# Performance work log

Hardware: AMD Instinct MI355X
Metric: run time of the kernel (lower is better)

Reference implementation:

```python
import jax, jax.numpy as jnp
import numpy as np

K = 3
STRIDE = 1
PAD = 1


def setup_inputs() -> dict:
    key = jax.random.key(0)
    k1, k2, k3 = jax.random.split(key, 3)
    N, C, H, W = 4, 256, 64, 64
    outC = 256
    x = jax.random.normal(k1, (N, C, H, W), dtype=jnp.float32)
    # offset/mask conv params (torch inits these to 0; small random makes the test nontrivial)
    conv_offset_w = jax.random.normal(k2, (3 * K * K, C, K, K), dtype=jnp.float32) * 0.01
    conv_offset_b = jnp.zeros((3 * K * K,), dtype=jnp.float32)
    # xavier-normal scale for dcn weight
    fan = C * K * K + outC * K * K
    dcn_weight = jax.random.normal(k3, (outC, C, K, K), dtype=jnp.float32) * np.float32(np.sqrt(2.0 / fan))
    return {"x": x, "conv_offset_w": conv_offset_w, "conv_offset_b": conv_offset_b, "dcn_weight": dcn_weight}


def _dcn(x, w_off, b_off, dcn_weight):
    k, s, p = K, STRIDE, PAD
    N, C, H, W = x.shape
    outC = dcn_weight.shape[0]
    KK = k * k
    # offset/mask prediction conv
    om = jax.lax.conv_general_dilated(
        x, w_off, (s, s), [(p, p), (p, p)],
        dimension_numbers=("NCHW", "OIHW", "NCHW")) + b_off[None, :, None, None]
    offset = om[:, : 2 * KK]
    mask = jax.nn.sigmoid(om[:, 2 * KK:])
    oH = (H + 2 * p - (k - 1)) // s
    oW = (W + 2 * p - (k - 1)) // s
    # pad with an extra row/col at bottom-right so floor+1 indexing is in-bounds (as in torch code)
    px = jnp.pad(x, ((0, 0), (0, 0), (p, p + 1), (p, p + 1)))
    px = jnp.transpose(px, (0, 2, 3, 1))  # (N, H+2p+1, W+2p+1, C)
    offset = jnp.transpose(offset, (0, 2, 3, 1)).reshape(N, oH, oW, KK, 2)  # (...,(y,x))
    mask = jnp.transpose(mask, (0, 2, 3, 1))  # (N, oH, oW, KK)
    base_y = jnp.arange(oH, dtype=jnp.float32) * s + p
    base_x = jnp.arange(oW, dtype=jnp.float32) * s + p
    half = (k - 1) // 2
    inner_y = jnp.repeat(jnp.arange(k, dtype=jnp.float32) - half, k)  # kernel-tap y offsets
    inner_x = jnp.tile(jnp.arange(k, dtype=jnp.float32) - half, k)   # kernel-tap x offsets
    pos_y = base_y[None, :, None, None] + inner_y[None, None, None, :] + offset[..., 0]
    pos_x = base_x[None, None, :, None] + inner_x[None, None, None, :] + offset[..., 1]
    pos_y = jnp.clip(pos_y, 0.0, H + 2 * p - 1.0)
    pos_x = jnp.clip(pos_x, 0.0, W + 2 * p - 1.0)
    y1 = jnp.floor(pos_y)
    x1 = jnp.floor(pos_x)
    y1i = y1.astype(jnp.int32)
    x1i = x1.astype(jnp.int32)
    nidx = jnp.arange(N)[:, None, None, None]
    # bilinear gathers: each (N, oH, oW, KK, C)
    v1 = px[nidx, y1i, x1i]
    v2 = px[nidx, y1i, x1i + 1]
    v3 = px[nidx, y1i + 1, x1i]
    v4 = px[nidx, y1i + 1, x1i + 1]
    lh = (pos_y - y1)[..., None]
    lw = (pos_x - x1)[..., None]
    hh = 1.0 - lh
    hw = 1.0 - lw
    value = hh * hw * v1 + hh * lw * v2 + lh * hw * v3 + lh * lw * v4
    value = value * mask[..., None]  # modulated
    w = dcn_weight.reshape(outC, C, KK)
    # sum over in_C and kernel taps -> NCHW output
    out = jnp.einsum("nhwkc,ock->nohw", value, w)
    return out


def reference(x, conv_offset_w, conv_offset_b, dcn_weight):
    return _dcn(x, conv_offset_w, conv_offset_b, dcn_weight)
```

## Files before the change

kernel.cpp:

```cpp
#include <hip/hip_runtime.h>
#include <type_traits>


typedef __bf16 bf16x8 __attribute__((ext_vector_type(8)));
typedef float  f32x4  __attribute__((ext_vector_type(4)));
typedef unsigned short ushort8 __attribute__((ext_vector_type(8)));
typedef unsigned int   uint4v  __attribute__((ext_vector_type(4)));

#define XBF_OFF   0u
#define WREP_OFF  8388608u
#define WMAIN_OFF 8536064u
#define OM_OFF    9715712u

#define LGKM0_BAR() do { __builtin_amdgcn_s_waitcnt(0xC07F); __builtin_amdgcn_s_barrier(); } while (0)

template <int N> using ic = std::integral_constant<int, N>;

__device__ __forceinline__ unsigned short f2bf(float f) {
  unsigned int u = __float_as_uint(f);
  u += 0x7fffu + ((u >> 16) & 1u);
  return (unsigned short)(u >> 16);
}
__device__ __forceinline__ float bf2f(unsigned short h) {
  return __uint_as_float(((unsigned int)h) << 16);
}

__global__ __launch_bounds__(256) void k_pre(const float* __restrict__ x,
                                             const float* __restrict__ w_off,
                                             const float* __restrict__ dcn_w,
                                             unsigned short* __restrict__ xbf,
                                             unsigned short* __restrict__ wrep,
                                             unsigned short* __restrict__ wmain) {
  __shared__ float tile[32][65];
  __shared__ unsigned short lsh[2304];
  int b = blockIdx.x;
  int t = threadIdx.x;
  if (b < 2048) {
    int n  = b >> 9;
    int cb = (b >> 6) & 7;
    int xb = b & 63;
    int xx  = t & 63;
    int cc0 = t >> 6;
#pragma unroll
    for (int j = 0; j < 8; ++j) {
      int cc = cc0 + j * 4;
      tile[cc][xx] = x[((size_t)(n * 256 + cb * 32 + cc) << 12) + xb * 64 + xx];
    }
    __syncthreads();
    int ccw = t & 31;
    int xw0 = t >> 5;
#pragma unroll
    for (int j = 0; j < 8; ++j) {
      int xw = xw0 + j * 8;
      xbf[((size_t)((n << 12) + xb * 64 + xw)) * 256 + cb * 32 + ccw] = f2bf(tile[ccw][xw]);
    }
  } else {
    int ocb = b - 2048;
    const float* src;
    unsigned short* dst;
    int oc;
    if (ocb < 32) { oc = ocb; src = w_off; dst = wrep; }
    else          { oc = ocb - 32; src = dcn_w; dst = wmain; }
    if (ocb < 32 && oc >= 27) {
#pragma unroll
      for (int j = 0; j < 9; ++j) dst[oc * 2304 + j * 256 + t] = 0;
      return;
    }
    const float* base = src + (size_t)oc * 2304;
#pragma unroll
    for (int j = 0; j < 9; ++j) lsh[j * 256 + t] = f2bf(base[t * 9 + j]);
    __syncthreads();
#pragma unroll
    for (int j = 0; j < 9; ++j) dst[oc * 2304 + j * 256 + t] = lsh[j * 256 + t];
  }
}

__global__ __launch_bounds__(1024) void k_offconv(const unsigned short* __restrict__ xbf,
                                                  const unsigned short* __restrict__ wrep,
                                                  const float* __restrict__ bias,
                                                  float* __restrict__ om) {
  __shared__ __align__(16) unsigned short SHa[4][64 * 64];
  __shared__ __align__(16) unsigned short SHb[4][32 * 64];
  int t = threadIdx.x;
  int wave = t >> 6, lane = t & 63;
  int grp = wave >> 2, wv = wave & 3;
  int tg = t & 255;
  int bm = ((blockIdx.x & 7) << 5) + (blockIdx.x >> 3);
  int n = bm >> 6, oy = bm & 63;

  unsigned short* As = SHa[grp];
  unsigned short* Bs = SHb[grp];

  int arow = tg >> 2, acc4 = tg & 3;
  int brow = tg >> 3, bch = tg & 7;

  f32x4 acc0 = {0.f, 0.f, 0.f, 0.f};
  f32x4 acc1 = {0.f, 0.f, 0.f, 0.f};

  ushort8 av[2][2]; ushort8 bv[2];
  auto prefetch = [&](int ktg, auto slotc) {
    constexpr int slot = decltype(slotc)::value;
    int kk = ktg >> 2;
    int c0 = (ktg & 3) * 64;
    int dy = kk / 3 - 1, dx = kk % 3 - 1;
    int yy = oy + dy, xxg = arow + dx;
    bool ok = ((unsigned)yy < 64u) && ((unsigned)xxg < 64u);
    const unsigned short* p = xbf + (size_t)(((n * 64 + yy) * 64 + xxg) * 256 + c0 + acc4 * 16);
#pragma unroll
    for (int g = 0; g < 2; ++g)
      av[slot][g] = ok ? *(const ushort8*)(p + g * 8) : (ushort8){0,0,0,0,0,0,0,0};
    bv[slot] = *(const ushort8*)(wrep + (size_t)brow * 2304 + ktg * 64 + bch * 8);
  };

  int k0 = grp * 9;
  prefetch(k0, ic<0>{});
  prefetch(k0 + 1, ic<1>{});
  int mr = lane & 15, q = lane >> 4;

  auto step = [&](int kt, auto slotc) {
    constexpr int slot = decltype(slotc)::value;
    LGKM0_BAR();
#pragma unroll
    for (int g = 0; g < 2; ++g) {
      int ch = (acc4 * 2 + g) ^ (arow & 7);
      *(ushort8*)&As[arow * 64 + ch * 8] = av[slot][g];
    }
    { int ch = bch ^ (brow & 7);
      *(ushort8*)&Bs[brow * 64 + ch * 8] = bv[slot]; }
    if (kt + 2 < 9) prefetch(k0 + kt + 2, slotc);
    LGKM0_BAR();
#pragma unroll
    for (int kh = 0; kh < 2; ++kh) {
      int coff = ((q + kh * 4) ^ (mr & 7)) * 8;
      bf16x8 a  = *(const bf16x8*)&As[(wv * 16 + mr) * 64 + coff];
      bf16x8 b0 = *(const bf16x8*)&Bs[mr * 64 + coff];
      bf16x8 b1 = *(const bf16x8*)&Bs[(16 + mr) * 64 + coff];
      acc0 = __builtin_amdgcn_mfma_f32_16x16x32_bf16(a, b0, acc0, 0, 0, 0);
      acc1 = __builtin_amdgcn_mfma_f32_16x16x32_bf16(a, b1, acc1, 0, 0, 0);
    }
  };
  for (int kp = 0; kp < 4; ++kp) {
    step(2 * kp, ic<0>{});
    step(2 * kp + 1, ic<1>{});
  }
  step(8, ic<0>{});

  float* scratch = (float*)&SHa[0][0];
  __syncthreads();
  if (grp > 0) {
#pragma unroll
    for (int nt = 0; nt < 2; ++nt) {
      f32x4 a = nt ? acc1 : acc0;
#pragma unroll
      for (int rg = 0; rg < 4; ++rg)
        scratch[(grp - 1) * 2048 + (wv * 16 + q * 4 + rg) * 32 + nt * 16 + mr] = a[rg];
    }
  }
  __syncthreads();
  if (grp == 0) {
    int r0 = bm * 64;
#pragma unroll
    for (int nt = 0; nt < 2; ++nt) {
      f32x4 a = nt ? acc1 : acc0;
      int oc = nt * 16 + mr;
      float bvl = (oc < 27) ? bias[oc] : 0.f;
#pragma unroll
      for (int rg = 0; rg < 4; ++rg) {
        int pl = wv * 16 + q * 4 + rg;
        float v = a[rg] + bvl + scratch[pl * 32 + oc] +
                  scratch[2048 + pl * 32 + oc] + scratch[4096 + pl * 32 + oc];
        if (oc >= 18 && oc < 27) v = 1.f / (1.f + __expf(-v));
        om[(r0 + pl) * 32 + oc] = v;
      }
    }
  }
}

__global__ __launch_bounds__(768, 3) void k_gemm_fused(const unsigned short* __restrict__ xbf,
                                                       const float* __restrict__ om,
                                                       const unsigned short* __restrict__ wB,
                                                       float* __restrict__ out) {
  __shared__ __align__(16) unsigned short Ab[2][64 * 64];
  __shared__ __align__(16) unsigned short Bb[2][256 * 64];
  int t = threadIdx.x;
  int wave = t >> 6, lane = t & 63;
  int bmx = ((blockIdx.x & 7) << 5) + (blockIdx.x >> 3);
  int r0 = bmx * 64;

  if (wave < 4) {
    int wn = wave;
    int mr = lane & 15, q = lane >> 4;
    f32x4 acc[4][4];
#pragma unroll
    for (int mt = 0; mt < 4; ++mt)
#pragma unroll
      for (int nt = 0; nt < 4; ++nt) acc[mt][nt] = (f32x4){0.f, 0.f, 0.f, 0.f};

    for (int p = 0; p < 37; ++p) {
      if (p >= 1) {
        int buf = (p - 1) & 1;
#pragma unroll
        for (int kh = 0; kh < 2; ++kh) {
          int coff = ((q + kh * 4) ^ (mr & 7)) * 8;
          bf16x8 af[4], bfv[4];
#pragma unroll
          for (int mt = 0; mt < 4; ++mt)
            af[mt] = *(const bf16x8*)&Ab[buf][(mt * 16 + mr) * 64 + coff];
#pragma unroll
          for (int nt = 0; nt < 4; ++nt)
            bfv[nt] = *(const bf16x8*)&Bb[buf][(wn * 64 + nt * 16 + mr) * 64 + coff];
#pragma unroll
          for (int mt = 0; mt < 4; ++mt)
#pragma unroll
            for (int nt = 0; nt < 4; ++nt)
              acc[mt][nt] = __builtin_amdgcn_mfma_f32_16x16x32_bf16(af[mt], bfv[nt], acc[mt][nt], 0, 0, 0);
        }
      }
      LGKM0_BAR();
    }

#pragma unroll
    for (int mt = 0; mt < 4; ++mt)
#pragma unroll
      for (int nt = 0; nt < 4; ++nt) {
        int p = r0 + mt * 16 + q * 4;
        int o = wn * 64 + nt * 16 + mr;
        int nn = p >> 12, pyx = p & 4095;
        *(f32x4*)(out + ((size_t)(nn * 256 + o) << 12) + pyx) = acc[mt][nt];
      }
  } else {
    int pt = t - 256;
    int srow = pt >> 3, sch = (pt & 7) * 8;
    int r = r0 + srow;
    int n = r >> 12, yx = r & 4095, oy = yx >> 6, ox = yx & 63;
    const unsigned short* xb = xbf + (size_t)n * (4096 * 256);
    const float* omr = om + (size_t)r * 32;
    int wchA = (((pt & 7) ^ (srow & 7)) << 3);
    int prow = pt >> 1;
    int pc0 = (pt & 1) * 4;
    const unsigned short* Bg = wB + (size_t)prow * 2304 + pc0 * 8;
    int bsw0 = (((pc0 + 0) ^ (prow & 7)) << 3);
    int bsw1 = (((pc0 + 1) ^ (prow & 7)) << 3);
    int bsw2 = (((pc0 + 2) ^ (prow & 7)) << 3);
    int bsw3 = (((pc0 + 3) ^ (prow & 7)) << 3);

    float pv_y, pv_x, pv_m;
    float cw1, cw2, cw3, cw4;
    int a1, a2, a3, a4;
    float wbuf[2][4];
    ushort8 g1[2], g2[2], g3[2], g4[2];
    uint4v bvp[2][4];

    auto loadom = [&](int kk) {
      pv_y = omr[2 * kk]; pv_x = omr[2 * kk + 1]; pv_m = omr[18 + kk];
    };
    auto params = [&](int kk) {
      float py = (float)(oy + kk / 3) + pv_y;
      float px = (float)(ox + kk % 3) + pv_x;
      float m = pv_m;
      py = fminf(fmaxf(py, 0.f), 65.f);
      px = fminf(fmaxf(px, 0.f), 65.f);
      float fy = floorf(py), fx = floorf(px);
      float ly = py - fy, lx = px - fx;
      float hy = 1.f - ly, hx = 1.f - lx;
      int iy = (int)fy, ix = (int)fx;
      bool yv0 = (iy >= 1) && (iy <= 64);
      bool yv1 = (iy <= 63);
      bool xv0 = (ix >= 1) && (ix <= 64);
      bool xv1 = (ix <= 63);
      int y0 = min(max(iy - 1, 0), 63);
      int y1 = min(iy, 63);
      int x0 = min(max(ix - 1, 0), 63);
      int x1 = min(ix, 63);
      cw1 = (yv0 && xv0) ? hy * hx * m : 0.f;
      cw2 = (yv0 && xv1) ? hy * lx * m : 0.f;
      cw3 = (yv1 && xv0) ? ly * hx * m : 0.f;
      cw4 = (yv1 && xv1) ? ly * lx * m : 0.f;
      a1 = ((y0 << 6) + x0) * 256;
      a2 = ((y0 << 6) + x1) * 256;
      a3 = ((y1 << 6) + x0) * 256;
      a4 = ((y1 << 6) + x1) * 256;
    };

    auto issueA = [&](int ktg, auto slotc) {
      constexpr int slot = decltype(slotc)::value;
      wbuf[slot][0] = cw1; wbuf[slot][1] = cw2; wbuf[slot][2] = cw3; wbuf[slot][3] = cw4;
      int c = (ktg & 3) * 64 + sch;
      g1[slot] = *(const ushort8*)(xb + a1 + c);
      g2[slot] = *(const ushort8*)(xb + a2 + c);
      g3[slot] = *(const ushort8*)(xb + a3 + c);
      g4[slot] = *(const ushort8*)(xb + a4 + c);
    };
    auto issueB = [&](int ktg, auto slotc) {
      constexpr int slot = decltype(slotc)::value;
#pragma unroll
      for (int j = 0; j < 4; ++j)
        bvp[slot][j] = *(const uint4v*)(Bg + (size_t)ktg * 64 + j * 8);
    };

    loadom(0);
    params(0);
    loadom(1);
    issueA(0, ic<0>{});
    issueB(0, ic<0>{});

    auto pphase = [&](int p, auto slotc) {
      constexpr int slot = decltype(slotc)::value;
      if (p + 1 < 36) {
        if (((p + 1) & 3) == 0) {
          int kk = (p + 1) >> 2;
          params(kk);
          loadom(kk < 8 ? kk + 1 : 8);
        }
        issueA(p + 1, ic<1 - slot>{});
        issueB(p + 1, ic<1 - slot>{});
      }
      uint4v rs;
#pragma unroll
      for (int pp = 0; pp < 4; ++pp) {
        float va = wbuf[slot][0] * bf2f(g1[slot][2 * pp])     + wbuf[slot][1] * bf2f(g2[slot][2 * pp]) +
                   wbuf[slot][2] * bf2f(g3[slot][2 * pp])     + wbuf[slot][3] * bf2f(g4[slot][2 * pp]);
        float vb = wbuf[slot][0] * bf2f(g1[slot][2 * pp + 1]) + wbuf[slot][1] * bf2f(g2[slot][2 * pp + 1]) +
                   wbuf[slot][2] * bf2f(g3[slot][2 * pp + 1]) + wbuf[slot][3] * bf2f(g4[slot][2 * pp + 1]);
        unsigned ua = __float_as_uint(va) + 0x8000u;
        unsigned ub = __float_as_uint(vb) + 0x8000u;
        rs[pp] = __builtin_amdgcn_perm(ub, ua, 0x07060302u);
      }
      *(uint4v*)&Ab[slot][srow * 64 + wchA] = rs;
      *(uint4v*)&Bb[slot][prow * 64 + bsw0] = bvp[slot][0];
      *(uint4v*)&Bb[slot][prow * 64 + bsw1] = bvp[slot][1];
      *(uint4v*)&Bb[slot][prow * 64 + bsw2] = bvp[slot][2];
      *(uint4v*)&Bb[slot][prow * 64 + bsw3] = bvp[slot][3];
      LGKM0_BAR();
    };

    for (int pp = 0; pp < 18; ++pp) {
      pphase(2 * pp, ic<0>{});
      pphase(2 * pp + 1, ic<1>{});
    }
    LGKM0_BAR();
  }
}

extern "C" void kernel_launch(void* const* d_in, const int* in_sizes, int n_in,
                              void* d_out, int out_size, void* d_ws, size_t ws_size,
                              hipStream_t stream) {
  const float* x     = (const float*)d_in[0];
  const float* w_off = (const float*)d_in[1];
  const float* b_off = (const float*)d_in[2];
  const float* dcn_w = (const float*)d_in[3];
  float* out = (float*)d_out;
  char* ws = (char*)d_ws;
  unsigned short* xbf   = (unsigned short*)(ws + XBF_OFF);
  unsigned short* wrep  = (unsigned short*)(ws + WREP_OFF);
  unsigned short* wmain = (unsigned short*)(ws + WMAIN_OFF);
  float*          om    = (float*)(ws + OM_OFF);

  k_pre<<<2048 + 288, 256, 0, stream>>>(x, w_off, dcn_w, xbf, wrep, wmain);
  k_offconv<<<256, 1024, 0, stream>>>(xbf, wrep, b_off, om);
  k_gemm_fused<<<256, 768, 0, stream>>>(xbf, om, wmain, out);
}
```

Baseline: 126.8 us.

## Load DCN weights directly into MFMA registers from pre-swizzled global layout

The preprocessing kernel now writes the main DCN weight in a fragment-ordered layout, so each MFMA wave can load its B operands straight from global memory into registers, double-buffered one iteration ahead. This removes the B tile staging through LDS (the global load, LDS store and LDS reads) and frees 64 KB of shared memory. The compute side grows to 8 waves, each covering 32 output channels, and the block grows to 1024 threads. The trade-off is that every wave now reads weights from L2 with no sharing through LDS, and per-block register pressure rises.

```diff
diff --git a/kernel.cpp b/kernel.cpp
--- a/kernel.cpp
+++ b/kernel.cpp
@@ -56,22 +56,30 @@
     }
   } else {
     int ocb = b - 2048;
-    const float* src;
-    unsigned short* dst;
-    int oc;
-    if (ocb < 32) { oc = ocb; src = w_off; dst = wrep; }
-    else          { oc = ocb - 32; src = dcn_w; dst = wmain; }
-    if (ocb < 32 && oc >= 27) {
-#pragma unroll
-      for (int j = 0; j < 9; ++j) dst[oc * 2304 + j * 256 + t] = 0;
-      return;
-    }
-    const float* base = src + (size_t)oc * 2304;
-#pragma unroll
-    for (int j = 0; j < 9; ++j) lsh[j * 256 + t] = f2bf(base[t * 9 + j]);
-    __syncthreads();
-#pragma unroll
-    for (int j = 0; j < 9; ++j) dst[oc * 2304 + j * 256 + t] = lsh[j * 256 + t];
+    if (ocb < 32) {
+      int oc = ocb;
+      if (oc >= 27) {
+#pragma unroll
+        for (int j = 0; j < 9; ++j) wrep[oc * 2304 + j * 256 + t] = 0;
+        return;
+      }
+      const float* base = w_off + (size_t)oc * 2304;
+#pragma unroll
+      for (int j = 0; j < 9; ++j) lsh[j * 256 + t] = f2bf(base[t * 9 + j]);
+      __syncthreads();
+#pragma unroll
+      for (int j = 0; j < 9; ++j) wrep[oc * 2304 + j * 256 + t] = lsh[j * 256 + t];
+    } else {
+      int oc = ocb - 32;
+      const float* base = dcn_w + (size_t)oc * 2304;
+      int oco = ((oc >> 4) << 9) + (oc & 15) * 8;
+#pragma unroll
+      for (int j = 0; j < 9; ++j) {
+        int k = j * 256 + t;
+        wmain[((k >> 5) << 13) + oco + (((k >> 3) & 3) << 7) + (k & 7)] =
+            f2bf(base[t * 9 + j]);
+      }
+    }
   }
 }
 
@@ -176,80 +184,88 @@
   }
 }
 
-__global__ __launch_bounds__(768, 3) void k_gemm_fused(const unsigned short* __restrict__ xbf,
-                                                       const float* __restrict__ om,
-                                                       const unsigned short* __restrict__ wB,
-                                                       float* __restrict__ out) {
+__global__ __launch_bounds__(1024, 4) void k_gemm_fused(const unsigned short* __restrict__ xbf,
+                                                        const float* __restrict__ om,
+                                                        const unsigned short* __restrict__ wB,
+                                                        float* __restrict__ out) {
   __shared__ __align__(16) unsigned short Ab[2][64 * 64];
-  __shared__ __align__(16) unsigned short Bb[2][256 * 64];
   int t = threadIdx.x;
   int wave = t >> 6, lane = t & 63;
   int bmx = ((blockIdx.x & 7) << 5) + (blockIdx.x >> 3);
   int r0 = bmx * 64;
 
-  if (wave < 4) {
-    int wn = wave;
+  if (wave < 8) {
     int mr = lane & 15, q = lane >> 4;
-    f32x4 acc[4][4];
+    const unsigned short* Bg = wB + wave * 1024 + lane * 8;
+    f32x4 acc[4][2];
 #pragma unroll
     for (int mt = 0; mt < 4; ++mt)
 #pragma unroll
-      for (int nt = 0; nt < 4; ++nt) acc[mt][nt] = (f32x4){0.f, 0.f, 0.f, 0.f};
-
-    for (int p = 0; p < 37; ++p) {
-      if (p >= 1) {
-        int buf = (p - 1) & 1;
+      for (int nt = 0; nt < 2; ++nt) acc[mt][nt] = (f32x4){0.f, 0.f, 0.f, 0.f};
+
+    bf16x8 bfr[2][4];
+
+    auto citer = [&](int p, bool do_issue, bool do_mfma, auto islotc) {
+      constexpr int islot = decltype(islotc)::value;
+      constexpr int mslot = 1 - islot;
+      if (do_issue) {
+#pragma unroll
+        for (int kh = 0; kh < 2; ++kh)
+#pragma unroll
+          for (int nt = 0; nt < 2; ++nt)
+            bfr[islot][kh * 2 + nt] =
+                *(const bf16x8*)(Bg + (size_t)(p * 2 + kh) * 8192 + nt * 512);
+      }
+      if (do_mfma) {
 #pragma unroll
         for (int kh = 0; kh < 2; ++kh) {
           int coff = ((q + kh * 4) ^ (mr & 7)) * 8;
-          bf16x8 af[4], bfv[4];
+          bf16x8 af[4];
 #pragma unroll
           for (int mt = 0; mt < 4; ++mt)
-            af[mt] = *(const bf16x8*)&Ab[buf][(mt * 16 + mr) * 64 + coff];
-#pragma unroll
-          for (int nt = 0; nt < 4; ++nt)
-            bfv[nt] = *(const bf16x8*)&Bb[buf][(wn * 64 + nt * 16 + mr) * 64 + coff];
+            af[mt] = *(const bf16x8*)&Ab[mslot][(mt * 16 + mr) * 64 + coff];
 #pragma unroll
           for (int mt = 0; mt < 4; ++mt)
 #pragma unroll
-            for (int nt = 0; nt < 4; ++nt)
-              acc[mt][nt] = __builtin_amdgcn_mfma_f32_16x16x32_bf16(af[mt], bfv[nt], acc[mt][nt], 0, 0, 0);
+            for (int nt = 0; nt < 2; ++nt)
+              acc[mt][nt] = __builtin_amdgcn_mfma_f32_16x16x32_bf16(
+                  af[mt], bfr[mslot][kh * 2 + nt], acc[mt][nt], 0, 0, 0);
         }
       }
       LGKM0_BAR();
-    }
+    };
+
+    citer(0, true, false, ic<0>{});
+    citer(1, true, true,  ic<1>{});
+    for (int pp = 1; pp < 18; ++pp) {
+      citer(2 * pp,     true, true, ic<0>{});
+      citer(2 * pp + 1, true, true, ic<1>{});
+    }
+    citer(36, false, true, ic<0>{});
 
 #pragma unroll
     for (int mt = 0; mt < 4; ++mt)
 #pragma unroll
-      for (int nt = 0; nt < 4; ++nt) {
+      for (int nt = 0; nt < 2; ++nt) {
         int p = r0 + mt * 16 + q * 4;
-        int o = wn * 64 + nt * 16 + mr;
+        int o = wave * 32 + nt * 16 + mr;
         int nn = p >> 12, pyx = p & 4095;
         *(f32x4*)(out + ((size_t)(nn * 256 + o) << 12) + pyx) = acc[mt][nt];
       }
   } else {
-    int pt = t - 256;
+    int pt = t - 512;
     int srow = pt >> 3, sch = (pt & 7) * 8;
     int r = r0 + srow;
     int n = r >> 12, yx = r & 4095, oy = yx >> 6, ox = yx & 63;
     const unsigned short* xb = xbf + (size_t)n * (4096 * 256);
     const float* omr = om + (size_t)r * 32;
     int wchA = (((pt & 7) ^ (srow & 7)) << 3);
-    int prow = pt >> 1;
-    int pc0 = (pt & 1) * 4;
-    const unsigned short* Bg = wB + (size_t)prow * 2304 + pc0 * 8;
-    int bsw0 = (((pc0 + 0) ^ (prow & 7)) << 3);
-    int bsw1 = (((pc0 + 1) ^ (prow & 7)) << 3);
-    int bsw2 = (((pc0 + 2) ^ (prow & 7)) << 3);
-    int bsw3 = (((pc0 + 3) ^ (prow & 7)) << 3);
 
     float pv_y, pv_x, pv_m;
     float cw1, cw2, cw3, cw4;
     int a1, a2, a3, a4;
     float wbuf[2][4];
     ushort8 g1[2], g2[2], g3[2], g4[2];
-    uint4v bvp[2][4];
 
     auto loadom = [&](int kk) {
       pv_y = omr[2 * kk]; pv_x = omr[2 * kk + 1]; pv_m = omr[18 + kk];
@@ -291,18 +307,11 @@
       g3[slot] = *(const ushort8*)(xb + a3 + c);
       g4[slot] = *(const ushort8*)(xb + a4 + c);
     };
-    auto issueB = [&](int ktg, auto slotc) {
-      constexpr int slot = decltype(slotc)::value;
-#pragma unroll
-      for (int j = 0; j < 4; ++j)
-        bvp[slot][j] = *(const uint4v*)(Bg + (size_t)ktg * 64 + j * 8);
-    };
 
     loadom(0);
     params(0);
     loadom(1);
     issueA(0, ic<0>{});
-    issueB(0, ic<0>{});
 
     auto pphase = [&](int p, auto slotc) {
       constexpr int slot = decltype(slotc)::value;
@@ -313,7 +322,6 @@
           loadom(kk < 8 ? kk + 1 : 8);
         }
         issueA(p + 1, ic<1 - slot>{});
-        issueB(p + 1, ic<1 - slot>{});
       }
       uint4v rs;
 #pragma unroll
@@ -327,10 +335,6 @@
         rs[pp] = __builtin_amdgcn_perm(ub, ua, 0x07060302u);
       }
       *(uint4v*)&Ab[slot][srow * 64 + wchA] = rs;
-      *(uint4v*)&Bb[slot][prow * 64 + bsw0] = bvp[slot][0];
-      *(uint4v*)&Bb[slot][prow * 64 + bsw1] = bvp[slot][1];
-      *(uint4v*)&Bb[slot][prow * 64 + bsw2] = bvp[slot][2];
-      *(uint4v*)&Bb[slot][prow * 64 + bsw3] = bvp[slot][3];
       LGKM0_BAR();
     };
 
@@ -358,5 +362,5 @@
 
   k_pre<<<2048 + 288, 256, 0, stream>>>(x, w_off, dcn_w, xbf, wrep, wmain);
   k_offconv<<<256, 1024, 0, stream>>>(xbf, wrep, b_off, om);
-  k_gemm_fused<<<256, 768, 0, stream>>>(xbf, om, wmain, out);
-}
+  k_gemm_fused<<<256, 1024, 0, stream>>>(xbf, om, wmain, out);
+}
```

After: 121.2 us. -4.4%, faster.
